# Kernel optimization log

Measured on AMD Instinct MI355X. Metric: run time of the kernel, lower is better.

The kernel has to match this reference:

```python
import jax, jax.numpy as jnp
import numpy as np

T, H, F, E, K = 4096, 1024, 4096, 8, 2


def setup_inputs() -> dict:
    key = jax.random.key(0)
    ks = jax.random.split(key, 6)
    hidden_states = jax.random.normal(ks[0], (T, H), dtype=jnp.float32)
    expert_weights = jax.random.uniform(ks[1], (T, K), dtype=jnp.float32)
    selected_experts = jax.random.randint(ks[2], (T, K), 0, E, dtype=jnp.int64)
    W1 = 0.02 * jax.random.normal(ks[3], (E, H, F), dtype=jnp.float32)
    b1 = jnp.zeros((E, F), dtype=jnp.float32)
    W2 = 0.02 * jax.random.normal(ks[4], (E, F, H), dtype=jnp.float32)
    b2 = jnp.zeros((E, H), dtype=jnp.float32)
    return {"hidden_states": hidden_states, "expert_weights": expert_weights,
            "W1": W1, "b1": b1, "W2": W2, "b2": b2,
            "selected_experts": selected_experts}


def reference(hidden_states, expert_weights, W1, b1, W2, b2, selected_experts):
    # Combine weight per (token, expert): sum of routing weights over top-k
    # slots assigned to that expert; slots with expert_idx < 0 contribute 0.
    num_experts = W1.shape[0]
    onehot = (selected_experts[:, :, None] == jnp.arange(num_experts)[None, None, :])
    valid = (selected_experts >= 0)[:, :, None]
    cw = jnp.einsum('tk,tke->te', expert_weights,
                    (onehot & valid).astype(hidden_states.dtype))  # [T, E]

    out = jnp.zeros_like(hidden_states)
    for e in range(num_experts):  # small fixed expert count
        h = jax.nn.gelu(hidden_states @ W1[e] + b1[e], approximate=False)  # [T, F]
        y = h @ W2[e] + b2[e]                                              # [T, H]
        out = out + cw[:, e:e + 1] * y
    return out
```

## Files before the change

kernel.cpp:

```cpp
#include <hip/hip_runtime.h>
#include <hip/hip_bf16.h>

#define Td 4096
#define Hd 1024
#define Fd 4096
#define Ed 8
#define Rcap 9216

typedef __attribute__((ext_vector_type(8))) short bf16x8;
typedef __attribute__((ext_vector_type(4))) float f32x4;
typedef __attribute__((ext_vector_type(8))) unsigned short u16x8;

__device__ __forceinline__ unsigned short f32_to_bf16(float x) {
  unsigned int u = __float_as_uint(x);
  unsigned int r = (u + 0x7FFFu + ((u >> 16) & 1u)) >> 16;
  return (unsigned short)r;
}

__device__ __forceinline__ void gload_lds16(const unsigned short* g, unsigned short* l) {
  __builtin_amdgcn_global_load_lds(
      (const __attribute__((address_space(1))) unsigned int*)g,
      (__attribute__((address_space(3))) unsigned int*)l, 16, 0, 0);
}

__global__ __launch_bounds__(256) void cvt_bf16_kernel(const float* __restrict__ in,
                                                       unsigned short* __restrict__ outp, int n8) {
  int i = blockIdx.x * 256 + threadIdx.x;
  if (i >= n8) return;
  const float4* p = (const float4*)(in + (size_t)i * 8);
  float4 a = p[0], b = p[1];
  u16x8 o;
  o[0] = f32_to_bf16(a.x); o[1] = f32_to_bf16(a.y); o[2] = f32_to_bf16(a.z); o[3] = f32_to_bf16(a.w);
  o[4] = f32_to_bf16(b.x); o[5] = f32_to_bf16(b.y); o[6] = f32_to_bf16(b.z); o[7] = f32_to_bf16(b.w);
  *(u16x8*)(outp + (size_t)i * 8) = o;
}

__global__ __launch_bounds__(256) void transpose_cvt_kernel(const float* __restrict__ in,
                                                            unsigned short* __restrict__ outp,
                                                            int Rdm, int Cdm) {
  __shared__ float tile[64][68];
  int tilesR = Rdm >> 6, tilesC = Cdm >> 6;
  int per = tilesR * tilesC;
  int bid = blockIdx.x;
  int e = bid / per; int rem = bid - e * per;
  int tr = rem / tilesC; int tc = rem - tr * tilesC;
  int r0 = tr << 6, c0 = tc << 6;
  int tid = threadIdx.x;
  int rr = tid >> 2, cq = (tid & 3) << 4;
  const float* src = in + ((size_t)e * Rdm + r0 + rr) * Cdm + c0 + cq;
  float4 v0 = ((const float4*)src)[0];
  float4 v1 = ((const float4*)src)[1];
  float4 v2 = ((const float4*)src)[2];
  float4 v3 = ((const float4*)src)[3];
  *(float4*)&tile[rr][cq + 0]  = v0;
  *(float4*)&tile[rr][cq + 4]  = v1;
  *(float4*)&tile[rr][cq + 8]  = v2;
  *(float4*)&tile[rr][cq + 12] = v3;
  __syncthreads();
  u16x8 o0, o1;
#pragma unroll
  for (int j = 0; j < 8; j++) o0[j] = f32_to_bf16(tile[cq + j][rr]);
#pragma unroll
  for (int j = 0; j < 8; j++) o1[j] = f32_to_bf16(tile[cq + 8 + j][rr]);
  unsigned short* dst = outp + ((size_t)e * Cdm + c0 + rr) * Rdm + r0 + cq;
  *(u16x8*)dst = o0;
  *(u16x8*)(dst + 8) = o1;
}

__global__ void init_meta_kernel(int* cnt) {
  if (threadIdx.x < Ed) cnt[threadIdx.x] = 0;
}

__global__ __launch_bounds__(256) void route_kernel(const int* __restrict__ sel,
                                                    const float* __restrict__ ew,
                                                    int* cnt, int* idxT, float* wgtT) {
  int t = blockIdx.x * 256 + threadIdx.x;
  if (t >= Td) return;
  int e0 = sel[t * 2], e1 = sel[t * 2 + 1];
  float w0 = ew[t * 2], w1 = ew[t * 2 + 1];
  if (e0 == e1) { w0 += w1; e1 = -1; }
  if (e0 >= 0 && e0 < Ed) { int p = atomicAdd(&cnt[e0], 1); idxT[e0 * Td + p] = t; wgtT[e0 * Td + p] = w0; }
  if (e1 >= 0 && e1 < Ed) { int p = atomicAdd(&cnt[e1], 1); idxT[e1 * Td + p] = t; wgtT[e1 * Td + p] = w1; }
}

__global__ void scan_kernel(const int* cnt, int* off) {
  if (threadIdx.x == 0) {
    int acc = 0; off[0] = 0;
#pragma unroll
    for (int e = 0; e < Ed; e++) { acc += (cnt[e] + 127) & ~127; off[e + 1] = acc; }
  }
}

__global__ __launch_bounds__(256) void compact_kernel(const int* __restrict__ cnt,
                                                      const int* __restrict__ off,
                                                      const int* __restrict__ idxT,
                                                      const float* __restrict__ wgtT,
                                                      int* __restrict__ cidx,
                                                      float* __restrict__ cwgt) {
  int j = blockIdx.x * 256 + threadIdx.x;
  int e = j >> 12; int i = j & (Td - 1);
  int base = off[e], end = off[e + 1];
  int row = base + i;
  if (row < end) {
    if (i < cnt[e]) { cidx[row] = idxT[e * Td + i]; cwgt[row] = wgtT[e * Td + i]; }
    else            { cidx[row] = -1;               cwgt[row] = 0.f; }
  }
}

template <bool FIRST, int KD, int NC, int BN>
__global__ __launch_bounds__(256) void gemm_kernel(const unsigned short* __restrict__ Abase,
                                                   const unsigned short* __restrict__ Bt,
                                                   const float* __restrict__ bias,
                                                   const int* __restrict__ cidx,
                                                   const float* __restrict__ cwgt,
                                                   const int* __restrict__ off,
                                                   unsigned short* __restrict__ hbuf,
                                                   float* __restrict__ outp) {
  constexpr int NF = BN / 32;
  int row0 = blockIdx.x << 7;
  int tot = off[Ed];
  if (row0 >= tot) return;
  int e = 0;
  while (off[e + 1] <= row0) ++e;
  int n0 = blockIdx.y * BN;

  __shared__ unsigned short As[128][64];
  __shared__ unsigned short Bs[BN][64];

  const int tid = threadIdx.x;
  const int lane = tid & 63, w = tid >> 6;
  const int wr = w >> 1, wc = w & 1;
  const int fr = lane & 15, fk = (lane >> 4) << 3;

  const int sofs = (lane & 7) << 3;
  const unsigned short* aptr[4];
#pragma unroll
  for (int i = 0; i < 4; i++) {
    int ar = (w << 5) + (i << 3) + (lane >> 3);
    int t;
    if (FIRST) { t = cidx[row0 + ar]; if (t < 0) t = 0; }
    else       { t = row0 + ar; }
    aptr[i] = Abase + (size_t)t * KD + sofs;
  }
  const unsigned short* bptr[NF];
#pragma unroll
  for (int i = 0; i < NF; i++) {
    int br = w * (BN / 4) + (i << 3) + (lane >> 3);
    bptr[i] = Bt + ((size_t)e * NC + n0 + br) * KD + sofs;
  }
  unsigned short* alds = &As[0][0] + (w << 11);
  unsigned short* blds = &Bs[0][0] + w * (BN * 16);

  f32x4 acc[4][NF] = {};

  for (int k0 = 0; k0 < KD; k0 += 64) {
    __syncthreads();
#pragma unroll
    for (int i = 0; i < 4; i++)  gload_lds16(aptr[i] + k0, alds + (i << 9));
#pragma unroll
    for (int i = 0; i < NF; i++) gload_lds16(bptr[i] + k0, blds + (i << 9));
    __syncthreads();
#pragma unroll
    for (int ks = 0; ks < 64; ks += 32) {
      bf16x8 af[4], bg[NF];
#pragma unroll
      for (int mi = 0; mi < 4; mi++)
        af[mi] = *(const bf16x8*)&As[(wr << 6) + (mi << 4) + fr][ks + fk];
#pragma unroll
      for (int ni = 0; ni < NF; ni++)
        bg[ni] = *(const bf16x8*)&Bs[wc * (BN / 2) + (ni << 4) + fr][ks + fk];
#pragma unroll
      for (int mi = 0; mi < 4; mi++)
#pragma unroll
        for (int ni = 0; ni < NF; ni++)
          acc[mi][ni] = __builtin_amdgcn_mfma_f32_16x16x32_bf16(af[mi], bg[ni], acc[mi][ni], 0, 0, 0);
    }
  }

  float bv[NF];
#pragma unroll
  for (int ni = 0; ni < NF; ni++) bv[ni] = bias[e * NC + n0 + wc * (BN / 2) + (ni << 4) + fr];
#pragma unroll
  for (int mi = 0; mi < 4; mi++) {
#pragma unroll
    for (int r2 = 0; r2 < 4; r2++) {
      int row = row0 + (wr << 6) + (mi << 4) + ((lane >> 4) << 2) + r2;
      if (FIRST) {
#pragma unroll
        for (int ni = 0; ni < NF; ni++) {
          int col = n0 + wc * (BN / 2) + (ni << 4) + fr;
          float x = acc[mi][ni][r2] + bv[ni];
          float g = 0.5f * x * (1.0f + erff(x * 0.70710678118654752f));
          hbuf[(size_t)row * NC + col] = f32_to_bf16(g);
        }
      } else {
        int tdst = cidx[row];
        float cw = cwgt[row];
        if (tdst >= 0) {
#pragma unroll
          for (int ni = 0; ni < NF; ni++) {
            int col = n0 + wc * (BN / 2) + (ni << 4) + fr;
            atomicAdd(outp + (size_t)tdst * NC + col, cw * (acc[mi][ni][r2] + bv[ni]));
          }
        }
      }
    }
  }
}

extern "C" void kernel_launch(void* const* d_in, const int* in_sizes, int n_in,
                              void* d_out, int out_size, void* d_ws, size_t ws_size,
                              hipStream_t stream) {
  const float* hidden = (const float*)d_in[0];
  const float* ew     = (const float*)d_in[1];
  const float* W1     = (const float*)d_in[2];
  const float* b1     = (const float*)d_in[3];
  const float* W2     = (const float*)d_in[4];
  const float* b2     = (const float*)d_in[5];
  const int*   sel    = (const int*)d_in[6];
  float* outp = (float*)d_out;

  unsigned short* hbf  = (unsigned short*)d_ws;
  unsigned short* W1T  = hbf + (size_t)Td * Hd;
  unsigned short* W2T  = W1T + (size_t)Ed * Fd * Hd;
  unsigned short* hbuf = W2T + (size_t)Ed * Hd * Fd;
  int*   cnt  = (int*)(hbuf + (size_t)Rcap * Fd);
  int*   off  = cnt + 16;
  int*   idxT = off + 16;
  float* wgtT = (float*)(idxT + Ed * Td);
  int*   cidx = (int*)(wgtT + Ed * Td);
  float* cwgt = (float*)(cidx + Rcap);

  (void)hipMemsetAsync(d_out, 0, (size_t)Td * Hd * sizeof(float), stream);

  cvt_bf16_kernel<<<(Td * Hd / 8 + 255) / 256, 256, 0, stream>>>(hidden, hbf, Td * Hd / 8);
  transpose_cvt_kernel<<<Ed * (Hd / 64) * (Fd / 64), 256, 0, stream>>>(W1, W1T, Hd, Fd);
  transpose_cvt_kernel<<<Ed * (Fd / 64) * (Hd / 64), 256, 0, stream>>>(W2, W2T, Fd, Hd);

  init_meta_kernel<<<1, 64, 0, stream>>>(cnt);
  route_kernel<<<Td / 256, 256, 0, stream>>>(sel, ew, cnt, idxT, wgtT);
  scan_kernel<<<1, 64, 0, stream>>>(cnt, off);
  compact_kernel<<<Ed * Td / 256, 256, 0, stream>>>(cnt, off, idxT, wgtT, cidx, cwgt);

  gemm_kernel<true, Hd, Fd, 128><<<dim3(Rcap / 128, Fd / 128), 256, 0, stream>>>(
      hbf, W1T, b1, cidx, cwgt, off, hbuf, nullptr);
  gemm_kernel<false, Fd, Hd, 64><<<dim3(Rcap / 128, Hd / 64), 256, 0, stream>>>(
      hbuf, W2T, b2, cidx, cwgt, off, nullptr, outp);
}
```

Baseline: 692.2 us.

## Rewrite grouped GEMMs with 256x128 tiles, triple-buffered LDS, split-K, fused routing

Both expert GEMMs now use 512-thread blocks on 256x128 tiles, with a three-stage LDS ring fed by async global-to-LDS loads and an XOR swizzle to avoid bank conflicts. The MFMA phases are interleaved with fragment loads and raised wave priority, and the second GEMM is split over K into two slices that accumulate through atomics. The four routing kernels are merged into one single-block kernel, and expert padding rises to multiples of 256, which enlarges Rcap. The intent is better latency hiding and data reuse in the GEMMs and fewer launches, at the cost of more padded rows, double atomic traffic in the second GEMM, and a serial single-block routing step.

After: 658.8 us. -4.8%, faster.

```diff
diff --git a/kernel.cpp b/kernel.cpp
--- a/kernel.cpp
+++ b/kernel.cpp
@@ -5,7 +5,7 @@
 #define Hd 1024
 #define Fd 4096
 #define Ed 8
-#define Rcap 9216
+#define Rcap 10240
 
 typedef __attribute__((ext_vector_type(8))) short bf16x8;
 typedef __attribute__((ext_vector_type(4))) float f32x4;
@@ -67,140 +67,207 @@
   *(u16x8*)(dst + 8) = o1;
 }
 
-__global__ void init_meta_kernel(int* cnt) {
-  if (threadIdx.x < Ed) cnt[threadIdx.x] = 0;
-}
-
-__global__ __launch_bounds__(256) void route_kernel(const int* __restrict__ sel,
-                                                    const float* __restrict__ ew,
-                                                    int* cnt, int* idxT, float* wgtT) {
-  int t = blockIdx.x * 256 + threadIdx.x;
-  if (t >= Td) return;
-  int e0 = sel[t * 2], e1 = sel[t * 2 + 1];
-  float w0 = ew[t * 2], w1 = ew[t * 2 + 1];
-  if (e0 == e1) { w0 += w1; e1 = -1; }
-  if (e0 >= 0 && e0 < Ed) { int p = atomicAdd(&cnt[e0], 1); idxT[e0 * Td + p] = t; wgtT[e0 * Td + p] = w0; }
-  if (e1 >= 0 && e1 < Ed) { int p = atomicAdd(&cnt[e1], 1); idxT[e1 * Td + p] = t; wgtT[e1 * Td + p] = w1; }
-}
-
-__global__ void scan_kernel(const int* cnt, int* off) {
-  if (threadIdx.x == 0) {
+__global__ __launch_bounds__(1024) void route_all_kernel(const int* __restrict__ sel,
+                                                         const float* __restrict__ ew,
+                                                         int* __restrict__ idxT,
+                                                         float* __restrict__ wgtT,
+                                                         int* __restrict__ off_g,
+                                                         int* __restrict__ cidx,
+                                                         float* __restrict__ cwgt) {
+  __shared__ int cnt[Ed];
+  __shared__ int off[Ed + 1];
+  int tid = threadIdx.x;
+  if (tid < Ed) cnt[tid] = 0;
+  __syncthreads();
+  for (int t = tid; t < Td; t += 1024) {
+    int e0 = sel[2 * t], e1 = sel[2 * t + 1];
+    float w0 = ew[2 * t], w1 = ew[2 * t + 1];
+    if (e0 == e1) { w0 += w1; e1 = -1; }
+    if (e0 >= 0 && e0 < Ed) { int p = atomicAdd(&cnt[e0], 1); idxT[e0 * Td + p] = t; wgtT[e0 * Td + p] = w0; }
+    if (e1 >= 0 && e1 < Ed) { int p = atomicAdd(&cnt[e1], 1); idxT[e1 * Td + p] = t; wgtT[e1 * Td + p] = w1; }
+  }
+  __syncthreads();
+  if (tid == 0) {
     int acc = 0; off[0] = 0;
 #pragma unroll
-    for (int e = 0; e < Ed; e++) { acc += (cnt[e] + 127) & ~127; off[e + 1] = acc; }
-  }
-}
-
-__global__ __launch_bounds__(256) void compact_kernel(const int* __restrict__ cnt,
+    for (int e = 0; e < Ed; e++) { acc += (cnt[e] + 255) & ~255; off[e + 1] = acc; }
+  }
+  __syncthreads();
+  for (int j = tid; j < Ed * Td; j += 1024) {
+    int e = j >> 12, i = j & (Td - 1);
+    int row = off[e] + i;
+    if (row < off[e + 1]) {
+      if (i < cnt[e]) { cidx[row] = idxT[e * Td + i]; cwgt[row] = wgtT[e * Td + i]; }
+      else            { cidx[row] = -1;               cwgt[row] = 0.f; }
+    }
+  }
+  if (tid <= Ed) off_g[tid] = off[tid];
+}
+
+template <bool FIRST, int KD, int NC, int KSPLIT>
+__global__ __launch_bounds__(512, 2) void gemm_kernel(const unsigned short* __restrict__ Abase,
+                                                      const unsigned short* __restrict__ Bt,
+                                                      const float* __restrict__ bias,
+                                                      const int* __restrict__ cidx,
+                                                      const float* __restrict__ cwgt,
                                                       const int* __restrict__ off,
-                                                      const int* __restrict__ idxT,
-                                                      const float* __restrict__ wgtT,
-                                                      int* __restrict__ cidx,
-                                                      float* __restrict__ cwgt) {
-  int j = blockIdx.x * 256 + threadIdx.x;
-  int e = j >> 12; int i = j & (Td - 1);
-  int base = off[e], end = off[e + 1];
-  int row = base + i;
-  if (row < end) {
-    if (i < cnt[e]) { cidx[row] = idxT[e * Td + i]; cwgt[row] = wgtT[e * Td + i]; }
-    else            { cidx[row] = -1;               cwgt[row] = 0.f; }
-  }
-}
-
-template <bool FIRST, int KD, int NC, int BN>
-__global__ __launch_bounds__(256) void gemm_kernel(const unsigned short* __restrict__ Abase,
-                                                   const unsigned short* __restrict__ Bt,
-                                                   const float* __restrict__ bias,
-                                                   const int* __restrict__ cidx,
-                                                   const float* __restrict__ cwgt,
-                                                   const int* __restrict__ off,
-                                                   unsigned short* __restrict__ hbuf,
-                                                   float* __restrict__ outp) {
-  constexpr int NF = BN / 32;
-  int row0 = blockIdx.x << 7;
-  int tot = off[Ed];
+                                                      unsigned short* __restrict__ hbuf,
+                                                      float* __restrict__ outp) {
+  extern __shared__ unsigned short lds[];
+  constexpr int KLEN = KD / KSPLIT;
+  constexpr int NT = KLEN / 64;
+
+  const int row0 = blockIdx.x << 8;
+  const int tot = off[Ed];
   if (row0 >= tot) return;
   int e = 0;
   while (off[e + 1] <= row0) ++e;
-  int n0 = blockIdx.y * BN;
-
-  __shared__ unsigned short As[128][64];
-  __shared__ unsigned short Bs[BN][64];
+  const int n0 = blockIdx.y << 7;
+  const int kbase = blockIdx.z * KLEN;
 
   const int tid = threadIdx.x;
   const int lane = tid & 63, w = tid >> 6;
-  const int wr = w >> 1, wc = w & 1;
-  const int fr = lane & 15, fk = (lane >> 4) << 3;
-
-  const int sofs = (lane & 7) << 3;
+  const int wrow = w >> 2, wcol = w & 3;
+  const int fr = lane & 15;
+  const int fkb = (lane >> 4) << 4;
+
   const unsigned short* aptr[4];
 #pragma unroll
   for (int i = 0; i < 4; i++) {
-    int ar = (w << 5) + (i << 3) + (lane >> 3);
-    int t;
-    if (FIRST) { t = cidx[row0 + ar]; if (t < 0) t = 0; }
-    else       { t = row0 + ar; }
-    aptr[i] = Abase + (size_t)t * KD + sofs;
-  }
-  const unsigned short* bptr[NF];
-#pragma unroll
-  for (int i = 0; i < NF; i++) {
-    int br = w * (BN / 4) + (i << 3) + (lane >> 3);
-    bptr[i] = Bt + ((size_t)e * NC + n0 + br) * KD + sofs;
-  }
-  unsigned short* alds = &As[0][0] + (w << 11);
-  unsigned short* blds = &Bs[0][0] + w * (BN * 16);
-
-  f32x4 acc[4][NF] = {};
-
-  for (int k0 = 0; k0 < KD; k0 += 64) {
-    __syncthreads();
-#pragma unroll
-    for (int i = 0; i < 4; i++)  gload_lds16(aptr[i] + k0, alds + (i << 9));
-#pragma unroll
-    for (int i = 0; i < NF; i++) gload_lds16(bptr[i] + k0, blds + (i << 9));
-    __syncthreads();
-#pragma unroll
-    for (int ks = 0; ks < 64; ks += 32) {
-      bf16x8 af[4], bg[NF];
-#pragma unroll
-      for (int mi = 0; mi < 4; mi++)
-        af[mi] = *(const bf16x8*)&As[(wr << 6) + (mi << 4) + fr][ks + fk];
-#pragma unroll
-      for (int ni = 0; ni < NF; ni++)
-        bg[ni] = *(const bf16x8*)&Bs[wc * (BN / 2) + (ni << 4) + fr][ks + fk];
-#pragma unroll
-      for (int mi = 0; mi < 4; mi++)
-#pragma unroll
-        for (int ni = 0; ni < NF; ni++)
-          acc[mi][ni] = __builtin_amdgcn_mfma_f32_16x16x32_bf16(af[mi], bg[ni], acc[mi][ni], 0, 0, 0);
-    }
-  }
-
-  float bv[NF];
-#pragma unroll
-  for (int ni = 0; ni < NF; ni++) bv[ni] = bias[e * NC + n0 + wc * (BN / 2) + (ni << 4) + fr];
-#pragma unroll
-  for (int mi = 0; mi < 4; mi++) {
-#pragma unroll
-    for (int r2 = 0; r2 < 4; r2++) {
-      int row = row0 + (wr << 6) + (mi << 4) + ((lane >> 4) << 2) + r2;
-      if (FIRST) {
-#pragma unroll
-        for (int ni = 0; ni < NF; ni++) {
-          int col = n0 + wc * (BN / 2) + (ni << 4) + fr;
-          float x = acc[mi][ni][r2] + bv[ni];
+    int r = (i << 6) + (tid >> 3);
+    int kel = ((tid & 7) ^ (r & 7)) << 3;
+    int g;
+    if (FIRST) { g = cidx[row0 + r]; if (g < 0) g = 0; }
+    else       { g = row0 + r; }
+    aptr[i] = Abase + (size_t)g * KD + kbase + kel;
+  }
+  const unsigned short* bptr[2];
+#pragma unroll
+  for (int i = 0; i < 2; i++) {
+    int r = (i << 6) + (tid >> 3);
+    int kel = ((tid & 7) ^ (r & 7)) << 3;
+    bptr[i] = Bt + ((size_t)e * NC + n0 + r) * KD + kbase + kel;
+  }
+  unsigned short* ldsA = lds;
+  unsigned short* ldsB = lds + 49152;
+
+  f32x4 acc[8][2] = {};
+
+#define STAGE(t)                                                         \
+  {                                                                      \
+    int _b = (t) % 3;                                                    \
+    int _k0 = (t) << 6;                                                  \
+    unsigned short* _la = ldsA + (_b << 14) + (w << 9);                  \
+    unsigned short* _lb = ldsB + (_b << 13) + (w << 9);                  \
+    _Pragma("unroll")                                                    \
+    for (int _i = 0; _i < 4; _i++) gload_lds16(aptr[_i] + _k0, _la + (_i << 12)); \
+    _Pragma("unroll")                                                    \
+    for (int _i = 0; _i < 2; _i++) gload_lds16(bptr[_i] + _k0, _lb + (_i << 12)); \
+  }
+
+#define LDA(dst, buf, m, ks)                                                     \
+  {                                                                              \
+    int _r = (wrow << 7) + ((m) << 4) + fr;                                      \
+    int _p = (((ks) << 6) + fkb) ^ ((_r & 7) << 4);                              \
+    dst = *(const bf16x8*)(ldsA + ((buf) << 14) + (_r << 6) + (_p >> 1));        \
+  }
+#define LDB(dst, buf, nf, ks)                                                    \
+  {                                                                              \
+    int _r = (wcol << 5) + ((nf) << 4) + fr;                                     \
+    int _p = (((ks) << 6) + fkb) ^ ((_r & 7) << 4);                              \
+    dst = *(const bf16x8*)(ldsB + ((buf) << 13) + (_r << 6) + (_p >> 1));        \
+  }
+
+  STAGE(0);
+  if constexpr (NT > 1) {
+    STAGE(1);
+    asm volatile("s_waitcnt vmcnt(6)" ::: "memory");
+  } else {
+    asm volatile("s_waitcnt vmcnt(0)" ::: "memory");
+  }
+  __builtin_amdgcn_s_barrier();
+
+  for (int t = 0; t < NT; ++t) {
+    const int buf = t % 3;
+    bf16x8 bfr[2][2];
+#pragma unroll
+    for (int nf = 0; nf < 2; nf++)
+#pragma unroll
+      for (int ks = 0; ks < 2; ks++) LDB(bfr[nf][ks], buf, nf, ks);
+    bf16x8 afr[4][2];
+#pragma unroll
+    for (int m = 0; m < 4; m++)
+#pragma unroll
+      for (int ks = 0; ks < 2; ks++) LDA(afr[m][ks], buf, m, ks);
+    if (t + 2 < NT) STAGE(t + 2);
+    __builtin_amdgcn_s_barrier();
+    __builtin_amdgcn_s_setprio(1);
+#pragma unroll
+    for (int m = 0; m < 4; m++)
+#pragma unroll
+      for (int nf = 0; nf < 2; nf++)
+#pragma unroll
+        for (int ks = 0; ks < 2; ks++)
+          acc[m][nf] = __builtin_amdgcn_mfma_f32_16x16x32_bf16(afr[m][ks], bfr[nf][ks], acc[m][nf], 0, 0, 0);
+    __builtin_amdgcn_s_setprio(0);
+    __builtin_amdgcn_s_barrier();
+#pragma unroll
+    for (int m = 0; m < 4; m++)
+#pragma unroll
+      for (int ks = 0; ks < 2; ks++) LDA(afr[m][ks], buf, m + 4, ks);
+    __builtin_amdgcn_s_barrier();
+    __builtin_amdgcn_s_setprio(1);
+#pragma unroll
+    for (int m = 0; m < 4; m++)
+#pragma unroll
+      for (int nf = 0; nf < 2; nf++)
+#pragma unroll
+        for (int ks = 0; ks < 2; ks++)
+          acc[m + 4][nf] = __builtin_amdgcn_mfma_f32_16x16x32_bf16(afr[m][ks], bfr[nf][ks], acc[m + 4][nf], 0, 0, 0);
+    __builtin_amdgcn_s_setprio(0);
+    if (t + 2 < NT) { asm volatile("s_waitcnt vmcnt(6)" ::: "memory"); }
+    else            { asm volatile("s_waitcnt vmcnt(0)" ::: "memory"); }
+    __builtin_amdgcn_s_barrier();
+  }
+#undef STAGE
+#undef LDA
+#undef LDB
+
+  if (FIRST) {
+    float bv[2];
+#pragma unroll
+    for (int nf = 0; nf < 2; nf++) bv[nf] = bias[e * NC + n0 + (wcol << 5) + (nf << 4) + fr];
+#pragma unroll
+    for (int m = 0; m < 8; m++) {
+#pragma unroll
+      for (int r2 = 0; r2 < 4; r2++) {
+        int row = row0 + (wrow << 7) + (m << 4) + ((lane >> 4) << 2) + r2;
+#pragma unroll
+        for (int nf = 0; nf < 2; nf++) {
+          int col = n0 + (wcol << 5) + (nf << 4) + fr;
+          float x = acc[m][nf][r2] + bv[nf];
           float g = 0.5f * x * (1.0f + erff(x * 0.70710678118654752f));
           hbuf[(size_t)row * NC + col] = f32_to_bf16(g);
         }
-      } else {
+      }
+    }
+  } else {
+    float bv[2];
+#pragma unroll
+    for (int nf = 0; nf < 2; nf++)
+      bv[nf] = (blockIdx.z == 0) ? bias[e * NC + n0 + (wcol << 5) + (nf << 4) + fr] : 0.f;
+#pragma unroll
+    for (int m = 0; m < 8; m++) {
+#pragma unroll
+      for (int r2 = 0; r2 < 4; r2++) {
+        int row = row0 + (wrow << 7) + (m << 4) + ((lane >> 4) << 2) + r2;
         int tdst = cidx[row];
         float cw = cwgt[row];
         if (tdst >= 0) {
 #pragma unroll
-          for (int ni = 0; ni < NF; ni++) {
-            int col = n0 + wc * (BN / 2) + (ni << 4) + fr;
-            atomicAdd(outp + (size_t)tdst * NC + col, cw * (acc[mi][ni][r2] + bv[ni]));
+          for (int nf = 0; nf < 2; nf++) {
+            int col = n0 + (wcol << 5) + (nf << 4) + fr;
+            atomicAdd(outp + (size_t)tdst * NC + col, cw * (acc[m][nf][r2] + bv[nf]));
           }
         }
       }
@@ -224,12 +291,17 @@
   unsigned short* W1T  = hbf + (size_t)Td * Hd;
   unsigned short* W2T  = W1T + (size_t)Ed * Fd * Hd;
   unsigned short* hbuf = W2T + (size_t)Ed * Hd * Fd;
-  int*   cnt  = (int*)(hbuf + (size_t)Rcap * Fd);
-  int*   off  = cnt + 16;
-  int*   idxT = off + 16;
+  int*   idxT = (int*)(hbuf + (size_t)Rcap * Fd);
   float* wgtT = (float*)(idxT + Ed * Td);
-  int*   cidx = (int*)(wgtT + Ed * Td);
+  int*   off  = (int*)(wgtT + Ed * Td);
+  int*   cidx = off + 16;
   float* cwgt = (float*)(cidx + Rcap);
+
+  constexpr int LDS_BYTES = 147456;
+  (void)hipFuncSetAttribute((const void*)gemm_kernel<true, Hd, Fd, 1>,
+                            hipFuncAttributeMaxDynamicSharedMemorySize, LDS_BYTES);
+  (void)hipFuncSetAttribute((const void*)gemm_kernel<false, Fd, Hd, 2>,
+                            hipFuncAttributeMaxDynamicSharedMemorySize, LDS_BYTES);
 
   (void)hipMemsetAsync(d_out, 0, (size_t)Td * Hd * sizeof(float), stream);
 
@@ -237,13 +309,10 @@
   transpose_cvt_kernel<<<Ed * (Hd / 64) * (Fd / 64), 256, 0, stream>>>(W1, W1T, Hd, Fd);
   transpose_cvt_kernel<<<Ed * (Fd / 64) * (Hd / 64), 256, 0, stream>>>(W2, W2T, Fd, Hd);
 
-  init_meta_kernel<<<1, 64, 0, stream>>>(cnt);
-  route_kernel<<<Td / 256, 256, 0, stream>>>(sel, ew, cnt, idxT, wgtT);
-  scan_kernel<<<1, 64, 0, stream>>>(cnt, off);
-  compact_kernel<<<Ed * Td / 256, 256, 0, stream>>>(cnt, off, idxT, wgtT, cidx, cwgt);
-
-  gemm_kernel<true, Hd, Fd, 128><<<dim3(Rcap / 128, Fd / 128), 256, 0, stream>>>(
+  route_all_kernel<<<1, 1024, 0, stream>>>(sel, ew, idxT, wgtT, off, cidx, cwgt);
+
+  gemm_kernel<true, Hd, Fd, 1><<<dim3(Rcap / 256, Fd / 128, 1), 512, LDS_BYTES, stream>>>(
       hbf, W1T, b1, cidx, cwgt, off, hbuf, nullptr);
-  gemm_kernel<false, Fd, Hd, 64><<<dim3(Rcap / 128, Hd / 64), 256, 0, stream>>>(
+  gemm_kernel<false, Fd, Hd, 2><<<dim3(Rcap / 256, Hd / 128, 2), 512, LDS_BYTES, stream>>>(
       hbuf, W2T, b2, cidx, cwgt, off, nullptr, outp);
 }
```
